# Kernel optimization log

Measured on AMD Instinct MI355X. Metric: run time of the kernel, lower is better.

## Reference

```python
import jax, jax.numpy as jnp
import numpy as np

N = 50000      # nodes
E = 500000     # edges
G = 8          # graphs in batch
H = 64         # latent width (message_passer out_channels)
FIN = 5        # raw node feature dim
MDIM = 3       # mask dim (last col = BC flag)
EF = 3         # edge feature dim
OUT = 4        # output dim
REPEATS = 4    # message passing repeats


def _mlp(h, w1, b1, w2, b2):
    return jnp.dot(jax.nn.relu(jnp.dot(h, w1) + b1), w2) + b2


def _seg_mean(v, idx, n):
    s = jax.ops.segment_sum(v, idx, num_segments=n)
    c = jax.ops.segment_sum(jnp.ones((v.shape[0], 1), v.dtype), idx, num_segments=n)
    return s / jnp.maximum(c, 1.0)


def _lin(k, fi, fo):
    return (jax.random.normal(k, (fi, fo), jnp.float32) / np.sqrt(fi),
            jnp.zeros((fo,), jnp.float32))


def setup_inputs() -> dict:
    key = jax.random.key(0)
    ks = jax.random.split(key, 16)
    x = jax.random.normal(ks[0], (N, FIN), jnp.float32)
    x_mask = jax.random.uniform(ks[1], (N, MDIM), jnp.float32)
    x_mask = x_mask.at[:, -1].set((x_mask[:, -1] > 0.9).astype(jnp.float32))
    edge_index = jax.random.randint(ks[2], (2, E), 0, N, jnp.int32)
    edge_attr = jax.random.normal(ks[3], (E, EF), jnp.float32)
    pos = jax.random.uniform(ks[4], (N, 2), jnp.float32)
    batch = jnp.sort(jax.random.randint(ks[5], (N,), 0, G, jnp.int32))
    enc_w1, enc_b1 = _lin(ks[6], FIN + MDIM, H)
    enc_w2, enc_b2 = _lin(ks[7], H, H)
    msg_w1, msg_b1 = _lin(ks[8], 2 * H + EF, H)
    msg_w2, msg_b2 = _lin(ks[9], H, H)
    upd_w1, upd_b1 = _lin(ks[10], 4 * H, H)
    upd_w2, upd_b2 = _lin(ks[11], H, H)
    dec_w1, dec_b1 = _lin(ks[12], H, H)
    dec_w2, dec_b2 = _lin(ks[13], H, OUT)
    return dict(x=x, x_mask=x_mask, edge_index=edge_index, edge_attr=edge_attr,
                pos=pos, batch=batch,
                enc_w1=enc_w1, enc_b1=enc_b1, enc_w2=enc_w2, enc_b2=enc_b2,
                msg_w1=msg_w1, msg_b1=msg_b1, msg_w2=msg_w2, msg_b2=msg_b2,
                upd_w1=upd_w1, upd_b1=upd_b1, upd_w2=upd_w2, upd_b2=upd_b2,
                dec_w1=dec_w1, dec_b1=dec_b1, dec_w2=dec_w2, dec_b2=dec_b2)


def reference(x, x_mask, edge_index, edge_attr, pos, batch,
              enc_w1, enc_b1, enc_w2, enc_b2,
              msg_w1, msg_b1, msg_w2, msg_b2,
              upd_w1, upd_b1, upd_w2, upd_b2,
              dec_w1, dec_b1, dec_w2, dec_b2):
    # x = concat([x, x_mask]); BC_idxs = x_mask[:, -1]
    bc = x_mask[:, -1:]                                   # [N,1] 0/1 BC flag
    h = _mlp(jnp.concatenate([x, x_mask], axis=1), enc_w1, enc_b1, enc_w2, enc_b2)
    # x_BC = scatter-mean of encoded BC nodes per graph (mask-weighted segment mean)
    bc_sum = jax.ops.segment_sum(h * bc, batch, num_segments=G)
    bc_cnt = jax.ops.segment_sum(bc, batch, num_segments=G)
    x_BC = bc_sum / jnp.maximum(bc_cnt, 1.0)              # [G,H]
    x_graph = _seg_mean(h, batch, G)                      # global_mean_pool [G,H]
    src, dst = edge_index[0], edge_index[1]
    for _ in range(REPEATS):
        # message: MLP over [x_src, x_dst, edge_attr], scatter-mean to dst
        m = _mlp(jnp.concatenate([h[src], h[dst], edge_attr], axis=1),
                 msg_w1, msg_b1, msg_w2, msg_b2)          # [E,H]
        agg = _seg_mean(m, dst, N)                        # [N,H]
        # node update conditioned on global and BC context, residual
        h = h + _mlp(jnp.concatenate([h, agg, x_graph[batch], x_BC[batch]], axis=1),
                     upd_w1, upd_b1, upd_w2, upd_b2)
        x_graph = _seg_mean(h, batch, G)                  # refreshed each repeat
    return _mlp(h, dec_w1, dec_b1, dec_w2, dec_b2)        # [N,OUT]
```

## Files before the change

### kernel.cpp

```cpp
#include <hip/hip_runtime.h>
#include <hip/hip_bf16.h>

#define NN 50000
#define EE 500000
#define GG 8
#define NB 196

#define SCALE_A 65536.0f
#define INV_SCALE_A (1.0f/65536.0f)
#define SCALE_G 16777216.0f
#define INV_SCALE_G (1.0f/16777216.0f)

using short8 = __attribute__((ext_vector_type(8))) short;
using f32x16 = __attribute__((ext_vector_type(16))) float;

__device__ __forceinline__ float4 ld4(const float* p){ return *reinterpret_cast<const float4*>(p); }

__device__ __forceinline__ short f2b(float f){
  union { __hip_bfloat16 b; short s; } u;
  u.b = __float2bfloat16(f);
  return u.s;
}

__global__ __launch_bounds__(256) void k_count(const int* __restrict__ dst, int* __restrict__ cnt){
  int e = blockIdx.x*256 + threadIdx.x;
  if (e < EE) atomicAdd(&cnt[dst[e]], 1);
}

__global__ __launch_bounds__(256) void k_scanA(const int* __restrict__ cnt, int* __restrict__ bsum){
  __shared__ int s[256];
  int t = threadIdx.x;
  int i = blockIdx.x*256 + t;
  s[t] = (i < NN) ? cnt[i] : 0;
  __syncthreads();
  for (int o=128;o>0;o>>=1){ if (t<o) s[t]+=s[t+o]; __syncthreads(); }
  if (t==0) bsum[blockIdx.x] = s[0];
}

__global__ __launch_bounds__(256) void k_scanB(const int* __restrict__ bsum, int* __restrict__ boff){
  __shared__ int s[256];
  int t = threadIdx.x;
  s[t] = (t < NB) ? bsum[t] : 0;
  __syncthreads();
  for (int o=1;o<256;o<<=1){
    int u = (t>=o) ? s[t-o] : 0;
    __syncthreads();
    s[t] += u;
    __syncthreads();
  }
  if (t < NB) boff[t] = (t==0) ? 0 : s[t-1];
}

__global__ __launch_bounds__(256) void k_scanC_prep(const int* __restrict__ cnt, const int* __restrict__ boff,
                                               int* __restrict__ offs,
                                               float* __restrict__ inv, const int* __restrict__ batch,
                                               const float* __restrict__ xm,
                                               float* __restrict__ ncnt, float* __restrict__ bccnt){
  __shared__ int s[256];
  __shared__ float lc[GG], lb[GG];
  int t = threadIdx.x;
  int i = blockIdx.x*256 + t;
  if (t < GG){ lc[t]=0.f; lb[t]=0.f; }
  int v = (i < NN) ? cnt[i] : 0;
  s[t] = v;
  __syncthreads();
  for (int o=1;o<256;o<<=1){
    int u = (t>=o) ? s[t-o] : 0;
    __syncthreads();
    s[t] += u;
    __syncthreads();
  }
  if (i < NN){
    offs[i] = boff[blockIdx.x] + s[t] - v;
    inv[i] = 1.0f / fmaxf((float)v, 1.0f);
    int g = batch[i];
    atomicAdd(&lc[g], 1.0f);
    atomicAdd(&lb[g], xm[i*3+2]);
  }
  __syncthreads();
  if (t < GG){ atomicAdd(&ncnt[t], lc[t]); atomicAdd(&bccnt[t], lb[t]); }
}

__global__ __launch_bounds__(256) void k_prep(const int* __restrict__ cnt, float* __restrict__ inv,
                       const int* __restrict__ batch, const float* __restrict__ xm,
                       float* __restrict__ ncnt, float* __restrict__ bccnt){
  __shared__ float lc[GG], lb[GG];
  int t = threadIdx.x;
  if (t < GG){ lc[t]=0.f; lb[t]=0.f; }
  __syncthreads();
  int i = blockIdx.x*256 + t;
  if (i < NN){
    inv[i] = 1.0f / fmaxf((float)cnt[i], 1.0f);
    int g = batch[i];
    atomicAdd(&lc[g], 1.0f);
    atomicAdd(&lb[g], xm[i*3+2]);
  }
  __syncthreads();
  if (t < GG){ atomicAdd(&ncnt[t], lc[t]); atomicAdd(&bccnt[t], lb[t]); }
}

__global__ __launch_bounds__(256) void k_scat1(const int* __restrict__ dst, int* __restrict__ offs,
                                               int* __restrict__ perm){
  int e = blockIdx.x*256 + threadIdx.x;
  if (e >= EE) return;
  int d = dst[e];
  int pos = atomicAdd(&offs[d], 1);
  perm[pos] = e;
}

__global__ __launch_bounds__(256) void k_scat2(const int* __restrict__ perm,
                                               const int* __restrict__ src, const int* __restrict__ dst,
                                               const float* __restrict__ ea,
                                               int* __restrict__ srcs_s, int* __restrict__ dsts_s,
                                               short* __restrict__ ea16){
  int i = blockIdx.x*256 + threadIdx.x;
  if (i >= EE) return;
  int e = perm[i];
  srcs_s[i] = src[e];
  dsts_s[i] = dst[e];
  int lo = ((int)(unsigned short)f2b(ea[(size_t)e*3+0])) |
           (((int)(unsigned short)f2b(ea[(size_t)e*3+1])) << 16);
  int hi = ((int)(unsigned short)f2b(ea[(size_t)e*3+2]));
  int2 v; v.x = lo; v.y = hi;
  *(int2*)(ea16 + (size_t)i*4) = v;
}

__device__ __forceinline__ void packone(const float* __restrict__ w, int Kreal, int idx, short* __restrict__ out){
  int k = idx >> 6, n = idx & 63;
  float v = (k < Kreal) ? w[k*64 + n] : 0.f;
  int ks = k >> 4, kl = k & 15;
  int lane = (n & 31) + 32*(kl >> 3);
  int e = kl & 7;
  out[(ks*2 + (n>>5))*512 + lane*8 + e] = f2b(v);
}

__global__ __launch_bounds__(256) void k_wpack(
    const float* __restrict__ mw1, const float* __restrict__ mw2,
    const float* __restrict__ uw1, const float* __restrict__ uw2,
    short* __restrict__ mw1p, short* __restrict__ mw2p,
    short* __restrict__ uw1p, short* __restrict__ uw2p){
  int gid = blockIdx.x*256 + threadIdx.x;
  int stride = gridDim.x*256;
  for (int i=gid; i<144*64; i+=stride) packone(mw1, 131, i, mw1p);
  for (int i=gid; i<64*64;  i+=stride) packone(mw2, 64,  i, mw2p);
  for (int i=gid; i<256*64; i+=stride) packone(uw1, 256, i, uw1p);
  for (int i=gid; i<64*64;  i+=stride) packone(uw2, 64,  i, uw2p);
}

__global__ __launch_bounds__(256) void k_enc(
    const float* __restrict__ x, const float* __restrict__ xm,
    const float* __restrict__ w1, const float* __restrict__ b1,
    const float* __restrict__ w2, const float* __restrict__ b2,
    float* __restrict__ h, short* __restrict__ h16){
  __shared__ float w1s[8*64];
  __shared__ float w2s[64*64];
  __shared__ float b1s[64], b2s[64];
  __shared__ float ols[4][64][17];
  int t = threadIdx.x;
  for (int i=t;i<8*64;i+=256) w1s[i]=w1[i];
  for (int i=t;i<64*64;i+=256) w2s[i]=w2[i];
  if (t<64){ b1s[t]=b1[t]; b2s[t]=b2[t]; }
  __syncthreads();
  const int w = t >> 6, lane = t & 63;
  const int base_w = blockIdx.x*256 + w*64;
  const int n = base_w + lane;
  const int nc = (n < NN) ? n : (NN-1);
  float in[8];
  #pragma unroll
  for (int k=0;k<5;k++) in[k] = x[nc*5+k];
  #pragma unroll
  for (int k=0;k<3;k++) in[5+k] = xm[nc*3+k];
  float hid[64];
  #pragma unroll
  for (int o=0;o<64;o++){
    float a = b1s[o];
    #pragma unroll
    for (int k=0;k<8;k++) a += in[k]*w1s[k*64+o];
    hid[o] = fmaxf(a, 0.f);
  }
  for (int c=0;c<4;c++){
    float a[16];
    #pragma unroll
    for (int j=0;j<16;j++) a[j] = b2s[c*16+j];
    for (int k=0;k<64;k++){
      float hv = hid[k];
      #pragma unroll
      for (int j=0;j<16;j++) a[j] += hv * w2s[k*64 + c*16 + j];
    }
    #pragma unroll
    for (int j=0;j<16;j++) ols[w][lane][j] = a[j];
    __syncthreads();
    #pragma unroll
    for (int p=0;p<4;p++){
      int nd = p*16 + (lane>>2);
      int jj = lane & 3;
      int ng = base_w + nd;
      if (ng < NN){
        float4 v = make_float4(ols[w][nd][jj*4+0], ols[w][nd][jj*4+1],
                               ols[w][nd][jj*4+2], ols[w][nd][jj*4+3]);
        *(float4*)(h + (size_t)ng*64 + c*16 + jj*4) = v;
      }
    }
    #pragma unroll
    for (int p=0;p<2;p++){
      int nd = p*32 + (lane>>1);
      int jj = (lane & 1)*8;
      int ng = base_w + nd;
      if (ng < NN){
        short8 s;
        #pragma unroll
        for (int q=0;q<8;q++) s[q] = f2b(ols[w][nd][jj+q]);
        *(short8*)(h16 + (size_t)ng*64 + c*16 + jj) = s;
      }
    }
    __syncthreads();
  }
}

__global__ __launch_bounds__(256) void k_gred(
    const float* __restrict__ h, const int* __restrict__ batch,
    const float* __restrict__ xm,
    unsigned long long* __restrict__ xg_sum, unsigned long long* __restrict__ xbc_sum, int withBC){
  __shared__ float ls[4][GG][64];
  __shared__ float lb[4][GG][64];
  int t = threadIdx.x;
  int d = t & 63, grp = t >> 6;
  for (int g=0; g<GG; g++){ ls[grp][g][d]=0.f; lb[grp][g][d]=0.f; }
  __syncthreads();
  for (int i = blockIdx.x*4 + grp; i < NN; i += gridDim.x*4){
    int g = batch[i];
    float v = h[(size_t)i*64 + d];
    ls[grp][g][d] += v;
    if (withBC) lb[grp][g][d] += v * xm[i*3+2];
  }
  __syncthreads();
  if (t < 64){
    for (int g=0; g<GG; g++){
      float s = ls[0][g][d]+ls[1][g][d]+ls[2][g][d]+ls[3][g][d];
      atomicAdd(&xg_sum[g*64+d], (unsigned long long)(long long)llrintf(s*SCALE_G));
    }
  } else if (withBC && t < 128){
    int dd = t & 63;
    for (int g=0; g<GG; g++){
      float s = lb[0][g][dd]+lb[1][g][dd]+lb[2][g][dd]+lb[3][g][dd];
      atomicAdd(&xbc_sum[g*64+dd], (unsigned long long)(long long)llrintf(s*SCALE_G));
    }
  }
}

__global__ void k_gfin(unsigned long long* __restrict__ xg_sum, const unsigned long long* __restrict__ xbc_sum,
                       const float* __restrict__ ncnt, const float* __restrict__ bccnt,
                       short* __restrict__ xg16, short* __restrict__ xbc16, int withBC){
  int t = threadIdx.x;
  int g = t >> 6;
  float sg = (float)(long long)xg_sum[t] * INV_SCALE_G;
  xg16[t] = f2b(sg / fmaxf(ncnt[g], 1.f));
  xg_sum[t] = 0;
  if (withBC){
    float sb = (float)(long long)xbc_sum[t] * INV_SCALE_G;
    xbc16[t] = f2b(sb / fmaxf(bccnt[g], 1.f));
  }
}

__global__ __launch_bounds__(256) void k_msg_s(
    const short* __restrict__ h16,
    const int* __restrict__ srcs_s, const int* __restrict__ dsts_s,
    const short* __restrict__ ea16,
    const short* __restrict__ w1p, const float* __restrict__ b1,
    const short* __restrict__ w2p, const float* __restrict__ b2,
    int* __restrict__ agg){
  __shared__ int buf[4][2304];
  const int t = threadIdx.x;
  const int w = t >> 6, lane = t & 63;
  const int r = lane & 31, khalf = lane >> 5;
  const int base = blockIdx.x*256 + w*64;

  const int slot = base + lane;
  const int dl = (slot < EE) ? dsts_s[slot] : -1;

  const int eA = base + r, eB = base + 32 + r;
  const bool vA = eA < EE, vB = eB < EE;
  const int sA = vA ? srcs_s[eA] : 0;
  const int sB = vB ? srcs_s[eB] : 0;
  int dA = __shfl(dl, r);        if (dA < 0) dA = 0;
  int dB = __shfl(dl, 32 + r);   if (dB < 0) dB = 0;

  short8 a0[9], a1[9];
  #pragma unroll
  for (int ks=0;ks<4;ks++){
    a0[ks]   = *(const short8*)(h16 + (long)sA*64 + ks*16 + khalf*8);
    a1[ks]   = *(const short8*)(h16 + (long)sB*64 + ks*16 + khalf*8);
  }
  #pragma unroll
  for (int ks=0;ks<4;ks++){
    a0[4+ks] = *(const short8*)(h16 + (long)dA*64 + ks*16 + khalf*8);
    a1[4+ks] = *(const short8*)(h16 + (long)dB*64 + ks*16 + khalf*8);
  }
  {
    short8 z0, z1;
    #pragma unroll
    for (int j=0;j<8;j++){ z0[j]=0; z1[j]=0; }
    if (khalf == 0){
      if (vA){
        int2 v = *(const int2*)(ea16 + (size_t)eA*4);
        z0[0]=(short)v.x; z0[1]=(short)(v.x>>16); z0[2]=(short)v.y; z0[3]=(short)(v.y>>16);
      }
      if (vB){
        int2 v = *(const int2*)(ea16 + (size_t)eB*4);
        z1[0]=(short)v.x; z1[1]=(short)(v.x>>16); z1[2]=(short)v.y; z1[3]=(short)(v.y>>16);
      }
    }
    a0[8] = z0; a1[8] = z1;
  }

  float b1v0 = b1[r], b1v1 = b1[32 + r];
  f32x16 acc00, acc01, acc10, acc11;
  #pragma unroll
  for (int j=0;j<16;j++){ acc00[j]=b1v0; acc01[j]=b1v1; acc10[j]=b1v0; acc11[j]=b1v1; }

  const short8* w1f = (const short8*)w1p;
  #pragma unroll
  for (int ks=0; ks<9; ks++){
    short8 bf0 = w1f[(ks*2+0)*64 + lane];
    short8 bf1 = w1f[(ks*2+1)*64 + lane];
    acc00 = __builtin_amdgcn_mfma_f32_32x32x16_bf16(a0[ks], bf0, acc00, 0, 0, 0);
    acc01 = __builtin_amdgcn_mfma_f32_32x32x16_bf16(a0[ks], bf1, acc01, 0, 0, 0);
    acc10 = __builtin_amdgcn_mfma_f32_32x32x16_bf16(a1[ks], bf0, acc10, 0, 0, 0);
    acc11 = __builtin_amdgcn_mfma_f32_32x32x16_bf16(a1[ks], bf1, acc11, 0, 0, 0);
  }

  short* hw = (short*)&buf[w][0];
  #pragma unroll
  for (int reg=0; reg<16; reg++){
    int row = (reg&3) + 8*(reg>>2) + 4*khalf;
    hw[(row     )*72 + r     ] = f2b(fmaxf(acc00[reg], 0.f));
    hw[(row     )*72 + 32 + r] = f2b(fmaxf(acc01[reg], 0.f));
    hw[(row + 32)*72 + r     ] = f2b(fmaxf(acc10[reg], 0.f));
    hw[(row + 32)*72 + 32 + r] = f2b(fmaxf(acc11[reg], 0.f));
  }

  float b2v0 = b2[r], b2v1 = b2[32 + r];
  f32x16 c00, c01, c10, c11;
  #pragma unroll
  for (int j=0;j<16;j++){ c00[j]=b2v0; c01[j]=b2v1; c10[j]=b2v0; c11[j]=b2v1; }

  const short8* w2f = (const short8*)w2p;
  #pragma unroll
  for (int ks=0; ks<4; ks++){
    short8 p0 = *(const short8*)(hw + (r     )*72 + ks*16 + khalf*8);
    short8 p1 = *(const short8*)(hw + (32 + r)*72 + ks*16 + khalf*8);
    short8 bf0 = w2f[(ks*2+0)*64 + lane];
    short8 bf1 = w2f[(ks*2+1)*64 + lane];
    c00 = __builtin_amdgcn_mfma_f32_32x32x16_bf16(p0, bf0, c00, 0, 0, 0);
    c01 = __builtin_amdgcn_mfma_f32_32x32x16_bf16(p0, bf1, c01, 0, 0, 0);
    c10 = __builtin_amdgcn_mfma_f32_32x32x16_bf16(p1, bf0, c10, 0, 0, 0);
    c11 = __builtin_amdgcn_mfma_f32_32x32x16_bf16(p1, bf1, c11, 0, 0, 0);
  }

  int* mb = &buf[w][0];

  #pragma unroll
  for (int reg=0; reg<16; reg++){
    int row = (reg&3) + 8*(reg>>2) + 4*khalf;
    mb[row*65 + r     ] = __float2int_rn(c00[reg]*SCALE_A);
    mb[row*65 + 32 + r] = __float2int_rn(c01[reg]*SCALE_A);
  }
  {
    int cur = 0;
    while (cur < 32){
      int d = __shfl(dl, cur);
      unsigned long long diff = __ballot(dl != d);
      unsigned low = (unsigned)diff;
      unsigned rest = low & (0xFFFFFFFEu << cur);
      int end = rest ? (__ffs(rest) - 1) : 32;
      if (d >= 0){
        int s = 0;
        for (int rr=cur; rr<end; rr++) s += mb[rr*65 + lane];
        atomicAdd(&agg[(size_t)d*64 + lane], s);
      }
      cur = end;
    }
  }

  #pragma unroll
  for (int reg=0; reg<16; reg++){
    int row = (reg&3) + 8*(reg>>2) + 4*khalf;
    mb[row*65 + r     ] = __float2int_rn(c10[reg]*SCALE_A);
    mb[row*65 + 32 + r] = __float2int_rn(c11[reg]*SCALE_A);
  }
  {
    int cur = 0;
    while (cur < 32){
      int d = __shfl(dl, 32 + cur);
      unsigned long long diff = __ballot(dl != d);
      unsigned hi = (unsigned)(diff >> 32);
      unsigned rest = hi & (0xFFFFFFFEu << cur);
      int end = rest ? (__ffs(rest) - 1) : 32;
      if (d >= 0){
        int s = 0;
        for (int rr=cur; rr<end; rr++) s += mb[rr*65 + lane];
        atomicAdd(&agg[(size_t)d*64 + lane], s);
      }
      cur = end;
    }
  }
}

__global__ __launch_bounds__(256) void k_msg_atomic(
    const short* __restrict__ h16, const int* __restrict__ src, const int* __restrict__ dst,
    const float* __restrict__ ea,
    const short* __restrict__ w1p, const float* __restrict__ b1,
    const short* __restrict__ w2p, const float* __restrict__ b2,
    int* __restrict__ agg){
  __shared__ short hidT[4][64*72];
  const int t = threadIdx.x;
  const int w = t >> 6, lane = t & 63;
  const int r = lane & 31, khalf = lane >> 5;
  const int base = blockIdx.x*256 + w*64;
  const int eA = base + r, eB = base + 32 + r;
  const bool vA = eA < EE, vB = eB < EE;
  const int sA = vA ? src[eA] : 0, dA_ = vA ? dst[eA] : 0;
  const int sB = vB ? src[eB] : 0, dB_ = vB ? dst[eB] : 0;

  float b1v0 = b1[r], b1v1 = b1[32 + r];
  f32x16 acc00, acc01, acc10, acc11;
  #pragma unroll
  for (int j=0;j<16;j++){ acc00[j]=b1v0; acc01[j]=b1v1; acc10[j]=b1v0; acc11[j]=b1v1; }

  const short8* w1f = (const short8*)w1p;
  #pragma unroll
  for (int ks=0; ks<9; ks++){
    short8 a0, a1;
    if (ks < 8){
      long offA, offB;
      if (ks < 4){
        offA = (long)sA*64 + ks*16 + khalf*8;
        offB = (long)sB*64 + ks*16 + khalf*8;
      } else {
        offA = (long)dA_*64 + (ks-4)*16 + khalf*8;
        offB = (long)dB_*64 + (ks-4)*16 + khalf*8;
      }
      a0 = *(const short8*)(h16 + offA);
      a1 = *(const short8*)(h16 + offB);
    } else {
      #pragma unroll
      for (int j=0;j<8;j++){ a0[j]=0; a1[j]=0; }
      if (khalf == 0){
        if (vA){ a0[0]=f2b(ea[3*eA]); a0[1]=f2b(ea[3*eA+1]); a0[2]=f2b(ea[3*eA+2]); }
        if (vB){ a1[0]=f2b(ea[3*eB]); a1[1]=f2b(ea[3*eB+1]); a1[2]=f2b(ea[3*eB+2]); }
      }
    }
    short8 bf0 = w1f[(ks*2+0)*64 + lane];
    short8 bf1 = w1f[(ks*2+1)*64 + lane];
    acc00 = __builtin_amdgcn_mfma_f32_32x32x16_bf16(a0, bf0, acc00, 0, 0, 0);
    acc01 = __builtin_amdgcn_mfma_f32_32x32x16_bf16(a0, bf1, acc01, 0, 0, 0);
    acc10 = __builtin_amdgcn_mfma_f32_32x32x16_bf16(a1, bf0, acc10, 0, 0, 0);
    acc11 = __builtin_amdgcn_mfma_f32_32x32x16_bf16(a1, bf1, acc11, 0, 0, 0);
  }

  short* hw = &hidT[w][0];
  #pragma unroll
  for (int reg=0; reg<16; reg++){
    int row = (reg&3) + 8*(reg>>2) + 4*khalf;
    hw[(row     )*72 + r     ] = f2b(fmaxf(acc00[reg], 0.f));
    hw[(row     )*72 + 32 + r] = f2b(fmaxf(acc01[reg], 0.f));
    hw[(row + 32)*72 + r     ] = f2b(fmaxf(acc10[reg], 0.f));
    hw[(row + 32)*72 + 32 + r] = f2b(fmaxf(acc11[reg], 0.f));
  }

  float b2v0 = b2[r], b2v1 = b2[32 + r];
  f32x16 c00, c01, c10, c11;
  #pragma unroll
  for (int j=0;j<16;j++){ c00[j]=b2v0; c01[j]=b2v1; c10[j]=b2v0; c11[j]=b2v1; }

  const short8* w2f = (const short8*)w2p;
  #pragma unroll
  for (int ks=0; ks<4; ks++){
    short8 a0 = *(const short8*)(hw + (r     )*72 + ks*16 + khalf*8);
    short8 a1 = *(const short8*)(hw + (32 + r)*72 + ks*16 + khalf*8);
    short8 bf0 = w2f[(ks*2+0)*64 + lane];
    short8 bf1 = w2f[(ks*2+1)*64 + lane];
    c00 = __builtin_amdgcn_mfma_f32_32x32x16_bf16(a0, bf0, c00, 0, 0, 0);
    c01 = __builtin_amdgcn_mfma_f32_32x32x16_bf16(a0, bf1, c01, 0, 0, 0);
    c10 = __builtin_amdgcn_mfma_f32_32x32x16_bf16(a1, bf0, c10, 0, 0, 0);
    c11 = __builtin_amdgcn_mfma_f32_32x32x16_bf16(a1, bf1, c11, 0, 0, 0);
  }

  #pragma unroll
  for (int reg=0; reg<16; reg++){
    int row = (reg&3) + 8*(reg>>2) + 4*khalf;
    int e0r = base + row;
    int e1r = base + 32 + row;
    int d0 = __shfl(dA_, row);
    int d1 = __shfl(dB_, row);
    if (e0r < EE){
      atomicAdd(&agg[(size_t)d0*64 + r     ], __float2int_rn(c00[reg]*SCALE_A));
      atomicAdd(&agg[(size_t)d0*64 + 32 + r], __float2int_rn(c01[reg]*SCALE_A));
    }
    if (e1r < EE){
      atomicAdd(&agg[(size_t)d1*64 + r     ], __float2int_rn(c10[reg]*SCALE_A));
      atomicAdd(&agg[(size_t)d1*64 + 32 + r], __float2int_rn(c11[reg]*SCALE_A));
    }
  }
}

__global__ __launch_bounds__(256) void k_upd(
    float* __restrict__ h32, short* __restrict__ h16,
    int* __restrict__ agg, const float* __restrict__ inv,
    const int* __restrict__ batch,
    const short* __restrict__ xg16, const short* __restrict__ xbc16,
    const short* __restrict__ w1p, const float* __restrict__ b1,
    const short* __restrict__ w2p, const float* __restrict__ b2,
    unsigned long long* __restrict__ xg_sum, int withG){
  __shared__ short hidT[4][32*72];
  __shared__ unsigned long long gs[GG*64];
  const int t = threadIdx.x;
  for (int i=t; i<GG*64; i+=256) gs[i]=0;
  __syncthreads();

  const int w = t >> 6, lane = t & 63;
  const int r = lane & 31, khalf = lane >> 5;
  const int n0 = blockIdx.x*128 + w*32;
  const int n = n0 + r;
  const int nc = (n < NN) ? n : (NN-1);
  const int g = batch[nc];
  const float sc = inv[nc] * INV_SCALE_A;

  float b1v0 = b1[r], b1v1 = b1[32 + r];
  f32x16 a0acc, a1acc;
  #pragma unroll
  for (int j=0;j<16;j++){ a0acc[j]=b1v0; a1acc[j]=b1v1; }

  const short8* w1f = (const short8*)w1p;
  #pragma unroll
  for (int ks=0; ks<16; ks++){
    short8 a;
    int so = (ks & 3)*16 + khalf*8;
    if (ks < 4){
      a = *(const short8*)(h16 + (long)nc*64 + so);
    } else if (ks < 8){
      int4 i0 = *(const int4*)(agg + (long)nc*64 + so);
      int4 i1 = *(const int4*)(agg + (long)nc*64 + so + 4);
      if (n < NN){
        *(int4*)(agg + (long)nc*64 + so)     = make_int4(0,0,0,0);
        *(int4*)(agg + (long)nc*64 + so + 4) = make_int4(0,0,0,0);
      }
      a[0]=f2b((float)i0.x*sc); a[1]=f2b((float)i0.y*sc); a[2]=f2b((float)i0.z*sc); a[3]=f2b((float)i0.w*sc);
      a[4]=f2b((float)i1.x*sc); a[5]=f2b((float)i1.y*sc); a[6]=f2b((float)i1.z*sc); a[7]=f2b((float)i1.w*sc);
    } else if (ks < 12){
      a = *(const short8*)(xg16 + g*64 + so);
    } else {
      a = *(const short8*)(xbc16 + g*64 + so);
    }
    short8 bf0 = w1f[(ks*2+0)*64 + lane];
    short8 bf1 = w1f[(ks*2+1)*64 + lane];
    a0acc = __builtin_amdgcn_mfma_f32_32x32x16_bf16(a, bf0, a0acc, 0, 0, 0);
    a1acc = __builtin_amdgcn_mfma_f32_32x32x16_bf16(a, bf1, a1acc, 0, 0, 0);
  }

  short* hw = &hidT[w][0];
  #pragma unroll
  for (int reg=0; reg<16; reg++){
    int row = (reg&3) + 8*(reg>>2) + 4*khalf;
    hw[row*72 + r     ] = f2b(fmaxf(a0acc[reg], 0.f));
    hw[row*72 + 32 + r] = f2b(fmaxf(a1acc[reg], 0.f));
  }

  float b2v0 = b2[r], b2v1 = b2[32 + r];
  f32x16 c0, c1;
  #pragma unroll
  for (int j=0;j<16;j++){ c0[j]=b2v0; c1[j]=b2v1; }

  const short8* w2f = (const short8*)w2p;
  #pragma unroll
  for (int ks=0; ks<4; ks++){
    short8 a = *(const short8*)(hw + r*72 + ks*16 + khalf*8);
    short8 bf0 = w2f[(ks*2+0)*64 + lane];
    short8 bf1 = w2f[(ks*2+1)*64 + lane];
    c0 = __builtin_amdgcn_mfma_f32_32x32x16_bf16(a, bf0, c0, 0, 0, 0);
    c1 = __builtin_amdgcn_mfma_f32_32x32x16_bf16(a, bf1, c1, 0, 0, 0);
  }

  const bool doG = (withG != 0);
  const int g0 = __shfl(g, 0), g31 = __shfl(g, 31);
  const bool uni = (g0 == g31);
  long long s0 = 0, s1 = 0;
  #pragma unroll
  for (int reg=0; reg<16; reg++){
    int row = (reg&3) + 8*(reg>>2) + 4*khalf;
    int gg = __shfl(g, row);
    int nn = n0 + row;
    if (nn < NN){
      size_t i0 = (size_t)nn*64 + r;
      float v0 = h32[i0] + c0[reg];
      float v1 = h32[i0+32] + c1[reg];
      h32[i0] = v0;    h16[i0] = f2b(v0);
      h32[i0+32] = v1; h16[i0+32] = f2b(v1);
      if (doG){
        long long q0 = llrintf(v0*SCALE_G), q1 = llrintf(v1*SCALE_G);
        if (uni){ s0 += q0; s1 += q1; }
        else {
          atomicAdd(&gs[gg*64 + r     ], (unsigned long long)q0);
          atomicAdd(&gs[gg*64 + 32 + r], (unsigned long long)q1);
        }
      }
    }
  }
  if (doG && uni && (s0|s1)){
    atomicAdd(&gs[g0*64 + r     ], (unsigned long long)s0);
    atomicAdd(&gs[g0*64 + 32 + r], (unsigned long long)s1);
  }
  __syncthreads();
  if (doG){
    for (int i=t; i<GG*64; i+=256){
      unsigned long long v = gs[i];
      if (v) atomicAdd(&xg_sum[i], v);
    }
  }
}

__global__ __launch_bounds__(256) void k_dec(
    const float* __restrict__ h,
    const float* __restrict__ w1, const float* __restrict__ b1,
    const float* __restrict__ w2, const float* __restrict__ b2,
    float* __restrict__ out){
  __shared__ float w1s[64*64];
  __shared__ float w2s[64*4];
  __shared__ float b1s[64], b2s[4];
  int t=threadIdx.x;
  for (int i=t;i<64*64;i+=256) w1s[i]=w1[i];
  for (int i=t;i<256;i+=256) w2s[i]=w2[i];
  if (t<64) b1s[t]=b1[t];
  if (t<4) b2s[t]=b2[t];
  __syncthreads();
  int n = blockIdx.x*256+t;
  if (n>=NN) return;
  float xr[64];
  #pragma unroll
  for (int k=0;k<16;k++){
    float4 v = ld4(h + (size_t)n*64 + k*4);
    xr[k*4+0]=v.x; xr[k*4+1]=v.y; xr[k*4+2]=v.z; xr[k*4+3]=v.w;
  }
  float a0=b2s[0],a1=b2s[1],a2=b2s[2],a3=b2s[3];
  for (int o=0;o<64;o++){
    float a=b1s[o];
    #pragma unroll
    for (int k=0;k<64;k++) a += xr[k]*w1s[k*64+o];
    a = fmaxf(a,0.f);
    a0 += a*w2s[o*4+0]; a1 += a*w2s[o*4+1]; a2 += a*w2s[o*4+2]; a3 += a*w2s[o*4+3];
  }
  out[(size_t)n*4+0]=a0; out[(size_t)n*4+1]=a1; out[(size_t)n*4+2]=a2; out[(size_t)n*4+3]=a3;
}

extern "C" void kernel_launch(void* const* d_in, const int* in_sizes, int n_in,
                              void* d_out, int out_size, void* d_ws, size_t ws_size,
                              hipStream_t stream){
  const float* x   = (const float*)d_in[0];
  const float* xm  = (const float*)d_in[1];
  const int*   ei  = (const int*)d_in[2];
  const float* ea  = (const float*)d_in[3];
  const int* batch = (const int*)d_in[5];
  const float* enc_w1=(const float*)d_in[6],  *enc_b1=(const float*)d_in[7];
  const float* enc_w2=(const float*)d_in[8],  *enc_b2=(const float*)d_in[9];
  const float* msg_w1=(const float*)d_in[10], *msg_b1=(const float*)d_in[11];
  const float* msg_w2=(const float*)d_in[12], *msg_b2=(const float*)d_in[13];
  const float* upd_w1=(const float*)d_in[14], *upd_b1=(const float*)d_in[15];
  const float* upd_w2=(const float*)d_in[16], *upd_b2=(const float*)d_in[17];
  const float* dec_w1=(const float*)d_in[18], *dec_b1=(const float*)d_in[19];
  const float* dec_w2=(const float*)d_in[20], *dec_b2=(const float*)d_in[21];
  const int* srcp = ei;
  const int* dstp = ei + EE;

  char* ws = (char*)d_ws;
  float* h32     = (float*)(ws + 0);
  int*   agg     = (int*)  (ws + 12800000);
  short* h16     = (short*)(ws + 25600000);
  float* inv     = (float*)(ws + 32000000);
  int*   cnt     = (int*)  (ws + 32200000);
  unsigned long long* xg_sum  = (unsigned long long*)(ws + 32400000);
  unsigned long long* xbc_sum = (unsigned long long*)(ws + 32404096);
  float* ncnt    = (float*)(ws + 32408192);
  float* bccnt   = (float*)(ws + 32408224);
  short* xg16    = (short*)(ws + 32408256);
  short* xbc16   = (short*)(ws + 32409280);
  short* mw1p    = (short*)(ws + 32410304);
  short* mw2p    = (short*)(ws + 32428736);
  short* uw1p    = (short*)(ws + 32436928);
  short* uw2p    = (short*)(ws + 32469696);
  int*   offs    = (int*)  (ws + 32477888);
  int*   srcs_s  = (int*)  (ws + 32677888);
  int*   dsts_s  = (int*)  (ws + 34678784);
  short* ea16s   = (short*)(ws + 36679680);
  int*   bsum    = (int*)  (ws + 40681472);
  int*   boff    = (int*)  (ws + 40682272);
  int*   perm    = (int*)  (ws + 40683072);
  const size_t WS_NEED_SORT = 42683968;
  const int useSort = (ws_size >= WS_NEED_SORT) ? 1 : 0;

  hipMemsetAsync(ws + 32200000, 0, 208256, stream);
  hipMemsetAsync(agg, 0, 12800000, stream);
  k_wpack<<<34, 256, 0, stream>>>(msg_w1, msg_w2, upd_w1, upd_w2, mw1p, mw2p, uw1p, uw2p);
  k_count<<<(EE+255)/256, 256, 0, stream>>>(dstp, cnt);
  if (useSort){
    k_scanA<<<NB, 256, 0, stream>>>(cnt, bsum);
    k_scanB<<<1, 256, 0, stream>>>(bsum, boff);
    k_scanC_prep<<<NB, 256, 0, stream>>>(cnt, boff, offs, inv, batch, xm, ncnt, bccnt);
    k_scat1<<<(EE+255)/256, 256, 0, stream>>>(dstp, offs, perm);
    k_scat2<<<(EE+255)/256, 256, 0, stream>>>(perm, srcp, dstp, ea, srcs_s, dsts_s, ea16s);
  } else {
    k_prep<<<(NN+255)/256, 256, 0, stream>>>(cnt, inv, batch, xm, ncnt, bccnt);
  }
  k_enc<<<(NN+255)/256, 256, 0, stream>>>(x, xm, enc_w1, enc_b1, enc_w2, enc_b2, h32, h16);
  k_gred<<<512, 256, 0, stream>>>(h32, batch, xm, xg_sum, xbc_sum, 1);
  k_gfin<<<1, 512, 0, stream>>>(xg_sum, xbc_sum, ncnt, bccnt, xg16, xbc16, 1);

  for (int rp=0; rp<4; rp++){
    if (useSort){
      k_msg_s<<<(EE+255)/256, 256, 0, stream>>>(h16, srcs_s, dsts_s, ea16s, mw1p, msg_b1, mw2p, msg_b2, agg);
    } else {
      k_msg_atomic<<<(EE+255)/256, 256, 0, stream>>>(h16, srcp, dstp, ea, mw1p, msg_b1, mw2p, msg_b2, agg);
    }
    int withG = (rp < 3) ? 1 : 0;
    k_upd<<<(NN+127)/128, 256, 0, stream>>>(h32, h16, agg, inv, batch, xg16, xbc16, uw1p, upd_b1, uw2p, upd_b2, xg_sum, withG);
    if (withG) k_gfin<<<1, 512, 0, stream>>>(xg_sum, xbc_sum, ncnt, bccnt, xg16, xbc16, 0);
  }
  k_dec<<<(NN+255)/256, 256, 0, stream>>>(h32, dec_w1, dec_b1, dec_w2, dec_b2, (float*)d_out);
}
```

Before: 412.8 us.

## Fold graph-context finalize into message kernel, use single-wave blocks with XCD remap

The per-repeat k_gfin launch is removed on the sort path: block 0 of k_msg_s now finalizes the graph-mean and BC context vectors and zeroes the accumulator. k_msg_s and k_upd now run with 64-thread single-wave blocks, and k_msg_s maps block indices to edge tiles with an XCD-aware permutation so neighbouring edge tiles share an L2. The workspace is reordered so one memset clears agg, counts and global sums together. The aim is fewer launches and better cache locality. The cost is 4x more k_upd blocks, each zeroing and flushing a 4KB shared global-sum buffer with global atomics.

```diff
diff --git a/kernel.cpp b/kernel.cpp
--- a/kernel.cpp
+++ b/kernel.cpp
@@ -262,19 +262,40 @@
   }
 }
 
-__global__ __launch_bounds__(256) void k_msg_s(
+__global__ __launch_bounds__(64) void k_msg_s(
     const short* __restrict__ h16,
     const int* __restrict__ srcs_s, const int* __restrict__ dsts_s,
     const short* __restrict__ ea16,
     const short* __restrict__ w1p, const float* __restrict__ b1,
     const short* __restrict__ w2p, const float* __restrict__ b2,
-    int* __restrict__ agg){
-  __shared__ int buf[4][2304];
+    int* __restrict__ agg,
+    unsigned long long* __restrict__ xg_sum, const unsigned long long* __restrict__ xbc_sum,
+    const float* __restrict__ ncnt, const float* __restrict__ bccnt,
+    short* __restrict__ xg16, short* __restrict__ xbc16, int withBC){
+  __shared__ int buf[2304];
   const int t = threadIdx.x;
-  const int w = t >> 6, lane = t & 63;
+  if (blockIdx.x == 0){
+    for (int i=t; i<GG*64; i+=64){
+      int g = i >> 6;
+      float sg = (float)(long long)xg_sum[i] * INV_SCALE_G;
+      xg16[i] = f2b(sg / fmaxf(ncnt[g], 1.f));
+      xg_sum[i] = 0;
+      if (withBC){
+        float sb = (float)(long long)xbc_sum[i] * INV_SCALE_G;
+        xbc16[i] = f2b(sb / fmaxf(bccnt[g], 1.f));
+      }
+    }
+  }
+  {
+  }
+  const int nwg = gridDim.x;
+  const int q = nwg >> 3, rm = nwg & 7;
+  const int xcd = blockIdx.x & 7, idx = blockIdx.x >> 3;
+  const int wg = (xcd < rm ? xcd*(q+1) : rm*(q+1) + (xcd-rm)*q) + idx;
+  const int base = wg * 64;
+
+  const int lane = t;
   const int r = lane & 31, khalf = lane >> 5;
-  const int base = blockIdx.x*256 + w*64;
-
   const int slot = base + lane;
   const int dl = (slot < EE) ? dsts_s[slot] : -1;
 
@@ -329,7 +350,7 @@
     acc11 = __builtin_amdgcn_mfma_f32_32x32x16_bf16(a1[ks], bf1, acc11, 0, 0, 0);
   }
 
-  short* hw = (short*)&buf[w][0];
+  short* hw = (short*)&buf[0];
   #pragma unroll
   for (int reg=0; reg<16; reg++){
     int row = (reg&3) + 8*(reg>>2) + 4*khalf;
@@ -357,7 +378,7 @@
     c11 = __builtin_amdgcn_mfma_f32_32x32x16_bf16(p1, bf1, c11, 0, 0, 0);
   }
 
-  int* mb = &buf[w][0];
+  int* mb = &buf[0];
 
   #pragma unroll
   for (int reg=0; reg<16; reg++){
@@ -504,7 +525,7 @@
   }
 }
 
-__global__ __launch_bounds__(256) void k_upd(
+__global__ __launch_bounds__(64) void k_upd(
     float* __restrict__ h32, short* __restrict__ h16,
     int* __restrict__ agg, const float* __restrict__ inv,
     const int* __restrict__ batch,
@@ -512,15 +533,15 @@
     const short* __restrict__ w1p, const float* __restrict__ b1,
     const short* __restrict__ w2p, const float* __restrict__ b2,
     unsigned long long* __restrict__ xg_sum, int withG){
-  __shared__ short hidT[4][32*72];
+  __shared__ short hidT[32*72];
   __shared__ unsigned long long gs[GG*64];
   const int t = threadIdx.x;
-  for (int i=t; i<GG*64; i+=256) gs[i]=0;
-  __syncthreads();
-
-  const int w = t >> 6, lane = t & 63;
+  for (int i=t; i<GG*64; i+=64) gs[i]=0;
+  __syncthreads();
+
+  const int lane = t;
   const int r = lane & 31, khalf = lane >> 5;
-  const int n0 = blockIdx.x*128 + w*32;
+  const int n0 = blockIdx.x*32;
   const int n = n0 + r;
   const int nc = (n < NN) ? n : (NN-1);
   const int g = batch[nc];
@@ -558,7 +579,7 @@
     a1acc = __builtin_amdgcn_mfma_f32_32x32x16_bf16(a, bf1, a1acc, 0, 0, 0);
   }
 
-  short* hw = &hidT[w][0];
+  short* hw = hidT;
   #pragma unroll
   for (int reg=0; reg<16; reg++){
     int row = (reg&3) + 8*(reg>>2) + 4*khalf;
@@ -612,7 +633,7 @@
   }
   __syncthreads();
   if (doG){
-    for (int i=t; i<GG*64; i+=256){
+    for (int i=t; i<GG*64; i+=64){
       unsigned long long v = gs[i];
       if (v) atomicAdd(&xg_sum[i], v);
     }
@@ -674,13 +695,13 @@
   char* ws = (char*)d_ws;
   float* h32     = (float*)(ws + 0);
   int*   agg     = (int*)  (ws + 12800000);
-  short* h16     = (short*)(ws + 25600000);
-  float* inv     = (float*)(ws + 32000000);
-  int*   cnt     = (int*)  (ws + 32200000);
-  unsigned long long* xg_sum  = (unsigned long long*)(ws + 32400000);
-  unsigned long long* xbc_sum = (unsigned long long*)(ws + 32404096);
-  float* ncnt    = (float*)(ws + 32408192);
-  float* bccnt   = (float*)(ws + 32408224);
+  int*   cnt     = (int*)  (ws + 25600000);
+  unsigned long long* xg_sum  = (unsigned long long*)(ws + 25800000);
+  unsigned long long* xbc_sum = (unsigned long long*)(ws + 25804096);
+  float* ncnt    = (float*)(ws + 25808192);
+  float* bccnt   = (float*)(ws + 25808224);
+  short* h16     = (short*)(ws + 25808256);
+  float* inv     = (float*)(ws + 32208256);
   short* xg16    = (short*)(ws + 32408256);
   short* xbc16   = (short*)(ws + 32409280);
   short* mw1p    = (short*)(ws + 32410304);
@@ -697,8 +718,7 @@
   const size_t WS_NEED_SORT = 42683968;
   const int useSort = (ws_size >= WS_NEED_SORT) ? 1 : 0;
 
-  hipMemsetAsync(ws + 32200000, 0, 208256, stream);
-  hipMemsetAsync(agg, 0, 12800000, stream);
+  hipMemsetAsync(ws + 12800000, 0, 13008256, stream);
   k_wpack<<<34, 256, 0, stream>>>(msg_w1, msg_w2, upd_w1, upd_w2, mw1p, mw2p, uw1p, uw2p);
   k_count<<<(EE+255)/256, 256, 0, stream>>>(dstp, cnt);
   if (useSort){
@@ -712,17 +732,22 @@
   }
   k_enc<<<(NN+255)/256, 256, 0, stream>>>(x, xm, enc_w1, enc_b1, enc_w2, enc_b2, h32, h16);
   k_gred<<<512, 256, 0, stream>>>(h32, batch, xm, xg_sum, xbc_sum, 1);
-  k_gfin<<<1, 512, 0, stream>>>(xg_sum, xbc_sum, ncnt, bccnt, xg16, xbc16, 1);
-
-  for (int rp=0; rp<4; rp++){
-    if (useSort){
-      k_msg_s<<<(EE+255)/256, 256, 0, stream>>>(h16, srcs_s, dsts_s, ea16s, mw1p, msg_b1, mw2p, msg_b2, agg);
-    } else {
+
+  if (useSort){
+    for (int rp=0; rp<4; rp++){
+      k_msg_s<<<(EE+63)/64, 64, 0, stream>>>(h16, srcs_s, dsts_s, ea16s, mw1p, msg_b1, mw2p, msg_b2, agg,
+                                             xg_sum, xbc_sum, ncnt, bccnt, xg16, xbc16, (rp==0)?1:0);
+      int withG = (rp < 3) ? 1 : 0;
+      k_upd<<<(NN+31)/32, 64, 0, stream>>>(h32, h16, agg, inv, batch, xg16, xbc16, uw1p, upd_b1, uw2p, upd_b2, xg_sum, withG);
+    }
+  } else {
+    k_gfin<<<1, 512, 0, stream>>>(xg_sum, xbc_sum, ncnt, bccnt, xg16, xbc16, 1);
+    for (int rp=0; rp<4; rp++){
       k_msg_atomic<<<(EE+255)/256, 256, 0, stream>>>(h16, srcp, dstp, ea, mw1p, msg_b1, mw2p, msg_b2, agg);
-    }
-    int withG = (rp < 3) ? 1 : 0;
-    k_upd<<<(NN+127)/128, 256, 0, stream>>>(h32, h16, agg, inv, batch, xg16, xbc16, uw1p, upd_b1, uw2p, upd_b2, xg_sum, withG);
-    if (withG) k_gfin<<<1, 512, 0, stream>>>(xg_sum, xbc_sum, ncnt, bccnt, xg16, xbc16, 0);
+      int withG = (rp < 3) ? 1 : 0;
+      k_upd<<<(NN+31)/32, 64, 0, stream>>>(h32, h16, agg, inv, batch, xg16, xbc16, uw1p, upd_b1, uw2p, upd_b2, xg_sum, withG);
+      if (withG) k_gfin<<<1, 512, 0, stream>>>(xg_sum, xbc_sum, ncnt, bccnt, xg16, xbc16, 0);
+    }
   }
   k_dec<<<(NN+255)/256, 256, 0, stream>>>(h32, dec_w1, dec_b1, dec_w2, dec_b2, (float*)d_out);
 }
```

After: 404.8 us. Within noise of the previous version (-1.9%).
